# Kernel tuning notes

Hardware: AMD Instinct MI355X
Metric: run time of the kernel (lower is better)

## Reference

```python
import jax, jax.numpy as jnp
import numpy as np

# --- placement constants (mirror init_kwargs) ---
N = 500_000           # total nodes
M = 450_000           # movable nodes (first M)
NBX = 1024
NBY = 1024
XL = 0.0
YL = 0.0
BSX = 1.0
BSY = 1.0
K = 8                 # max bin span per axis for 'large' nodes (node size < 7*bin)


def setup_inputs() -> dict:
    key = jax.random.key(0)
    k1, k2, k3, k4, k5, k6 = jax.random.split(key, 6)
    # node centers strictly inside the die so large-node windows stay in range
    px = jax.random.uniform(k1, (N,), jnp.float32, 4.0, 1020.0)
    py = jax.random.uniform(k2, (N,), jnp.float32, 4.0, 1020.0)
    pos = jnp.concatenate([px, py])                      # [2N]
    potential_field = jax.random.normal(k3, (NBX, NBY), jnp.float32)
    rho_current = jax.random.uniform(k4, (NBX, NBY), jnp.float32, 0.1, 2.0)
    node_size_x = jax.random.uniform(k5, (N,), jnp.float32, 0.2, 6.0)
    node_size_y = jax.random.uniform(k6, (N,), jnp.float32, 0.2, 6.0)
    return {"pos": pos, "potential_field": potential_field,
            "rho_current": rho_current,
            "node_size_x": node_size_x, "node_size_y": node_size_y}


def _velocity_field(pot, hx, hy):
    # v = -grad(phi): 2nd-order central interior, 1st-order one-sided edges
    vx = -jnp.concatenate([(pot[1:2] - pot[0:1]) / hx,
                           (pot[2:] - pot[:-2]) / (2.0 * hx),
                           (pot[-1:] - pot[-2:-1]) / hx], axis=0)
    vy = -jnp.concatenate([(pot[:, 1:2] - pot[:, 0:1]) / hy,
                           (pot[:, 2:] - pot[:, :-2]) / (2.0 * hy),
                           (pot[:, -1:] - pot[:, -2:-1]) / hy], axis=1)
    return vx, vy


def _axis_window(center, size, lo, bs, nb):
    # per-node K-bin window of overlap lengths along one axis
    left = center - 0.5 * size
    right = center + 0.5 * size
    bmin = jnp.clip(jnp.floor((left - lo) / bs).astype(jnp.int32), 0, nb - 1)
    bmax = jnp.clip(jnp.floor((right - lo) / bs).astype(jnp.int32), 0, nb - 1)
    b = bmin[:, None] + jnp.arange(K, dtype=jnp.int32)        # [M,K]
    bin_left = lo + b.astype(jnp.float32) * bs
    ov = jnp.minimum(right[:, None], bin_left + bs) - jnp.maximum(left[:, None], bin_left)
    ov = jnp.where((b <= bmax[:, None]) & (ov > 0.0), ov, 0.0)
    return jnp.clip(b, 0, nb - 1), ov


def _interpolate_flux(pos, flux_x, flux_y, nsx, nsy):
    pos_x = pos[:N]
    pos_y = pos[N:]
    px = pos_x[:M]
    py = pos_y[:M]
    # --- bilinear path (small nodes) ---
    gx = (px - XL) / BSX
    gy = (py - YL) / BSY
    ix = jnp.clip(jnp.floor(gx).astype(jnp.int32), 0, NBX - 1)
    iy = jnp.clip(jnp.floor(gy).astype(jnp.int32), 0, NBY - 1)
    wx = jnp.clip(gx - ix.astype(jnp.float32), 0.0, 1.0)
    wy = jnp.clip(gy - iy.astype(jnp.float32), 0.0, 1.0)
    ix1 = jnp.clip(ix + 1, 0, NBX - 1)
    iy1 = jnp.clip(iy + 1, 0, NBY - 1)

    def bilerp(f):
        return ((1.0 - wx) * (1.0 - wy) * f[ix, iy] + wx * (1.0 - wy) * f[ix1, iy]
                + (1.0 - wx) * wy * f[ix, iy1] + wx * wy * f[ix1, iy1])

    bil_fx = bilerp(flux_x)
    bil_fy = bilerp(flux_y)
    # --- exact area-weighted path (large nodes), vectorized over K x K window ---
    w = nsx[:M]
    h = nsy[:M]
    bx, ox = _axis_window(px, w, XL, BSX, NBX)                # [M,K]
    by, oy = _axis_window(py, h, YL, BSY, NBY)                # [M,K]
    weights = ox[:, :, None] * oy[:, None, :]                 # [M,K,K] overlap areas
    fx_win = flux_x[bx[:, :, None], by[:, None, :]]           # [M,K,K]
    fy_win = flux_y[bx[:, :, None], by[:, None, :]]
    area = w * h
    safe_area = jnp.maximum(area, 1e-30)
    area_fx = jnp.where(area > 0.0, (fx_win * weights).sum((1, 2)) / safe_area, 0.0)
    area_fy = jnp.where(area > 0.0, (fy_win * weights).sum((1, 2)) / safe_area, 0.0)
    large = (w >= BSX) | (h >= BSY)
    gpx = jnp.where(large, area_fx, bil_fx)
    gpy = jnp.where(large, area_fy, bil_fy)
    grad_pos = jnp.zeros_like(pos)
    grad_pos = grad_pos.at[:M].set(gpx)
    grad_pos = grad_pos.at[N:N + M].set(gpy)
    return grad_pos


def reference(pos, potential_field, rho_current, node_size_x, node_size_y):
    vx, vy = _velocity_field(potential_field, BSX, BSY)
    bin_area = BSX * BSY
    energy = 0.5 * (rho_current * bin_area * (vx * vx + vy * vy)).sum().reshape(1)
    grad_pos = _interpolate_flux(pos, vx, vy, node_size_x, node_size_y)
    return energy, grad_pos
```

## Files before the change

kernel.cpp:

```cpp
#include <hip/hip_runtime.h>
#include <hip/hip_fp16.h>

#define NPART 500000
#define MPART 450000
#define NBXC 1024
#define NBYC 1024
#define KROW 7
#define NBLK_PART 1954

__global__ __launch_bounds__(256) void field_kernel(const float* __restrict__ pot,
                                                    const float* __restrict__ rho,
                                                    __half2* __restrict__ v,
                                                    float* __restrict__ partials) {
    const int idx = blockIdx.x * 256 + threadIdx.x;
    const int i  = idx >> 8;
    const int j4 = (idx & 255) << 2;

    const int ip = min(i + 1, NBXC - 1);
    const int im = max(i - 1, 0);
    const float sx = (ip - im == 2) ? 0.5f : 1.0f;

    const float4 c  = *reinterpret_cast<const float4*>(pot + i  * NBYC + j4);
    const float4 cu = *reinterpret_cast<const float4*>(pot + ip * NBYC + j4);
    const float4 cd = *reinterpret_cast<const float4*>(pot + im * NBYC + j4);
    const float  cl = pot[i * NBYC + max(j4 - 1, 0)];
    const float  cr = pot[i * NBYC + min(j4 + 4, NBYC - 1)];
    const float4 r4 = *reinterpret_cast<const float4*>(rho + i * NBYC + j4);

    const float vx0 = -(cu.x - cd.x) * sx;
    const float vx1 = -(cu.y - cd.y) * sx;
    const float vx2 = -(cu.z - cd.z) * sx;
    const float vx3 = -(cu.w - cd.w) * sx;

    const float vy0 = (j4 == 0)             ? -(c.y - c.x) : -(c.y - cl) * 0.5f;
    const float vy1 = -(c.z - c.x) * 0.5f;
    const float vy2 = -(c.w - c.y) * 0.5f;
    const float vy3 = (j4 + 3 == NBYC - 1)  ? -(c.w - c.z) : -(cr - c.z) * 0.5f;

    float4 st;
    st.x = __builtin_bit_cast(float, __floats2half2_rn(vx0, vy0));
    st.y = __builtin_bit_cast(float, __floats2half2_rn(vx1, vy1));
    st.z = __builtin_bit_cast(float, __floats2half2_rn(vx2, vy2));
    st.w = __builtin_bit_cast(float, __floats2half2_rn(vx3, vy3));
    *reinterpret_cast<float4*>(v + i * NBYC + j4) = st;

    float e = r4.x * (vx0 * vx0 + vy0 * vy0)
            + r4.y * (vx1 * vx1 + vy1 * vy1)
            + r4.z * (vx2 * vx2 + vy2 * vy2)
            + r4.w * (vx3 * vx3 + vy3 * vy3);
    #pragma unroll
    for (int off = 32; off > 0; off >>= 1) e += __shfl_down(e, off, 64);
    __shared__ float smem[4];
    const int lane = threadIdx.x & 63;
    const int wid  = threadIdx.x >> 6;
    if (lane == 0) smem[wid] = e;
    __syncthreads();
    if (threadIdx.x == 0) partials[blockIdx.x] = (smem[0] + smem[1]) + (smem[2] + smem[3]);
}

__global__ __launch_bounds__(256) void particle_kernel(const float* __restrict__ pos,
                                                       const float* __restrict__ nsx,
                                                       const float* __restrict__ nsy,
                                                       const __half2* __restrict__ v,
                                                       const float* __restrict__ partials,
                                                       float* __restrict__ out) {
    __shared__ float smem[4];

    if (blockIdx.x == NBLK_PART) {
        const int t = threadIdx.x;
        float e = (partials[t] + partials[t + 256]) + (partials[t + 512] + partials[t + 768]);
        #pragma unroll
        for (int off = 32; off > 0; off >>= 1) e += __shfl_down(e, off, 64);
        const int lane = t & 63;
        const int wid  = t >> 6;
        if (lane == 0) smem[wid] = e;
        __syncthreads();
        if (t == 0) out[0] = 0.5f * ((smem[0] + smem[1]) + (smem[2] + smem[3]));
        return;
    }

    const int i = blockIdx.x * 256 + threadIdx.x;
    if (i >= NPART) return;
    if (i >= MPART) {
        out[1 + i]         = 0.0f;
        out[1 + NPART + i] = 0.0f;
        return;
    }

    const float px = pos[i];
    const float py = pos[NPART + i];
    const float w  = nsx[i];
    const float h  = nsy[i];

    float gpx, gpy;
    const bool large = (w >= 1.0f) || (h >= 1.0f);
    if (!large) {
        int ix = min(max((int)floorf(px), 0), NBXC - 1);
        int iy = min(max((int)floorf(py), 0), NBYC - 1);
        const float wx = fminf(fmaxf(px - (float)ix, 0.0f), 1.0f);
        const float wy = fminf(fmaxf(py - (float)iy, 0.0f), 1.0f);
        const int ix1 = min(ix + 1, NBXC - 1);
        const int iy1 = min(iy + 1, NBYC - 1);
        const float2 f00 = __half22float2(v[ix  * NBYC + iy ]);
        const float2 f10 = __half22float2(v[ix1 * NBYC + iy ]);
        const float2 f01 = __half22float2(v[ix  * NBYC + iy1]);
        const float2 f11 = __half22float2(v[ix1 * NBYC + iy1]);
        const float w00 = (1.0f - wx) * (1.0f - wy);
        const float w10 = wx * (1.0f - wy);
        const float w01 = (1.0f - wx) * wy;
        const float w11 = wx * wy;
        gpx = w00 * f00.x + w10 * f10.x + w01 * f01.x + w11 * f11.x;
        gpy = w00 * f00.y + w10 * f10.y + w01 * f01.y + w11 * f11.y;
    } else {
        const float lx = px - 0.5f * w, rx = px + 0.5f * w;
        const float ly = py - 0.5f * h, ry = py + 0.5f * h;
        const int bminx = min(max((int)floorf(lx), 0), NBXC - 1);
        const int bmaxx = min(max((int)floorf(rx), 0), NBXC - 1);
        const int bminy = min(max((int)floorf(ly), 0), NBYC - 1);
        const int bmaxy = min(max((int)floorf(ry), 0), NBYC - 1);
        const int by0 = min(bminy & ~3, NBYC - 12);
        const int nax = bmaxx - bminx;
        const bool need3 = (bmaxy >= by0 + 8);

        float4 q[KROW][3];
        #pragma unroll
        for (int k = 0; k < KROW; ++k) {
            const int bx = bminx + min(k, nax);
            const float4* rp = reinterpret_cast<const float4*>(v + bx * NBYC + by0);
            q[k][0] = rp[0];
            q[k][1] = rp[1];
            q[k][2] = need3 ? rp[2] : make_float4(0.0f, 0.0f, 0.0f, 0.0f);
        }

        float oy[12];
        #pragma unroll
        for (int k = 0; k < 12; ++k) {
            const int b = by0 + k;
            const float bl = (float)b;
            float ov = fminf(ry, bl + 1.0f) - fmaxf(ly, bl);
            oy[k] = (b <= bmaxy && ov > 0.0f) ? ov : 0.0f;
        }
        float ox[KROW];
        #pragma unroll
        for (int k = 0; k < KROW; ++k) {
            const int b = bminx + k;
            const float bl = (float)b;
            float ov = fminf(rx, bl + 1.0f) - fmaxf(lx, bl);
            ox[k] = (b <= bmaxx && ov > 0.0f) ? ov : 0.0f;
        }

        float afx = 0.0f, afy = 0.0f;
        #pragma unroll
        for (int k = 0; k < KROW; ++k) {
            float sx = 0.0f, sy = 0.0f;
            #pragma unroll
            for (int r = 0; r < 3; ++r) {
                const float* qs = &q[k][r].x;
                #pragma unroll
                for (int e = 0; e < 4; ++e) {
                    const float2 f = __half22float2(__builtin_bit_cast(__half2, qs[e]));
                    sx += f.x * oy[r * 4 + e];
                    sy += f.y * oy[r * 4 + e];
                }
            }
            afx += sx * ox[k];
            afy += sy * ox[k];
        }
        const float inv = 1.0f / fmaxf(w * h, 1e-30f);
        gpx = afx * inv;
        gpy = afy * inv;
    }
    out[1 + i]         = gpx;
    out[1 + NPART + i] = gpy;
}

extern "C" void kernel_launch(void* const* d_in, const int* in_sizes, int n_in,
                              void* d_out, int out_size, void* d_ws, size_t ws_size,
                              hipStream_t stream) {
    const float* pos = (const float*)d_in[0];
    const float* pot = (const float*)d_in[1];
    const float* rho = (const float*)d_in[2];
    const float* nsx = (const float*)d_in[3];
    const float* nsy = (const float*)d_in[4];
    float* out = (float*)d_out;

    __half2* v      = (__half2*)d_ws;
    float* partials = (float*)((char*)d_ws + (size_t)NBXC * NBYC * sizeof(__half2));

    field_kernel<<<(NBXC * NBYC / 4) / 256, 256, 0, stream>>>(pot, rho, v, partials);
    particle_kernel<<<NBLK_PART + 1, 256, 0, stream>>>(pos, nsx, nsy, v, partials, out);
}
```

Baseline: 35.33 us.

## Store velocity field in 2x8 tiled layout and gather large-node windows by tile

The half2 velocity field is now written in a tiled layout where each 2-row by 8-column block is contiguous, and the field kernel processes 8 columns per thread, halving the block count and the partial-sum count. Large-node area interpolation loads whole 2x8 or 2x16 tiles per pair of x-rows and skips x-pairs with zero overlap, instead of reading 7 separate rows. The aim is better cache-line locality and fewer memory transactions for the windowed gathers. The trade-off is fetching wider aligned windows (up to 8x16) that include unused bins, plus extra index arithmetic for bilinear lookups.

Result: faster. 30.01 us (-15.0%).

```diff
diff --git a/kernel.cpp b/kernel.cpp
--- a/kernel.cpp
+++ b/kernel.cpp
@@ -5,49 +5,57 @@
 #define MPART 450000
 #define NBXC 1024
 #define NBYC 1024
-#define KROW 7
 #define NBLK_PART 1954
+#define NPARTIAL 512
+
+__device__ __forceinline__ int tidx(int x, int y) {
+    return ((((x >> 1) * 128 + (y >> 3)) << 4) + ((x & 1) << 3) + (y & 7));
+}
 
 __global__ __launch_bounds__(256) void field_kernel(const float* __restrict__ pot,
                                                     const float* __restrict__ rho,
                                                     __half2* __restrict__ v,
                                                     float* __restrict__ partials) {
     const int idx = blockIdx.x * 256 + threadIdx.x;
-    const int i  = idx >> 8;
-    const int j4 = (idx & 255) << 2;
-
-    const int ip = min(i + 1, NBXC - 1);
-    const int im = max(i - 1, 0);
+    const int x  = idx >> 7;
+    const int ty = idx & 127;
+    const int j0 = ty << 3;
+
+    const int ip = min(x + 1, NBXC - 1);
+    const int im = max(x - 1, 0);
     const float sx = (ip - im == 2) ? 0.5f : 1.0f;
 
-    const float4 c  = *reinterpret_cast<const float4*>(pot + i  * NBYC + j4);
-    const float4 cu = *reinterpret_cast<const float4*>(pot + ip * NBYC + j4);
-    const float4 cd = *reinterpret_cast<const float4*>(pot + im * NBYC + j4);
-    const float  cl = pot[i * NBYC + max(j4 - 1, 0)];
-    const float  cr = pot[i * NBYC + min(j4 + 4, NBYC - 1)];
-    const float4 r4 = *reinterpret_cast<const float4*>(rho + i * NBYC + j4);
-
-    const float vx0 = -(cu.x - cd.x) * sx;
-    const float vx1 = -(cu.y - cd.y) * sx;
-    const float vx2 = -(cu.z - cd.z) * sx;
-    const float vx3 = -(cu.w - cd.w) * sx;
-
-    const float vy0 = (j4 == 0)             ? -(c.y - c.x) : -(c.y - cl) * 0.5f;
-    const float vy1 = -(c.z - c.x) * 0.5f;
-    const float vy2 = -(c.w - c.y) * 0.5f;
-    const float vy3 = (j4 + 3 == NBYC - 1)  ? -(c.w - c.z) : -(cr - c.z) * 0.5f;
-
-    float4 st;
-    st.x = __builtin_bit_cast(float, __floats2half2_rn(vx0, vy0));
-    st.y = __builtin_bit_cast(float, __floats2half2_rn(vx1, vy1));
-    st.z = __builtin_bit_cast(float, __floats2half2_rn(vx2, vy2));
-    st.w = __builtin_bit_cast(float, __floats2half2_rn(vx3, vy3));
-    *reinterpret_cast<float4*>(v + i * NBYC + j4) = st;
-
-    float e = r4.x * (vx0 * vx0 + vy0 * vy0)
-            + r4.y * (vx1 * vx1 + vy1 * vy1)
-            + r4.z * (vx2 * vx2 + vy2 * vy2)
-            + r4.w * (vx3 * vx3 + vy3 * vy3);
+    const float4* pc = reinterpret_cast<const float4*>(pot + x  * NBYC + j0);
+    const float4* pu = reinterpret_cast<const float4*>(pot + ip * NBYC + j0);
+    const float4* pd = reinterpret_cast<const float4*>(pot + im * NBYC + j0);
+    const float4* pr = reinterpret_cast<const float4*>(rho + x  * NBYC + j0);
+    float c[8], u[8], d[8], r[8];
+    *reinterpret_cast<float4*>(c)     = pc[0]; *reinterpret_cast<float4*>(c + 4) = pc[1];
+    *reinterpret_cast<float4*>(u)     = pu[0]; *reinterpret_cast<float4*>(u + 4) = pu[1];
+    *reinterpret_cast<float4*>(d)     = pd[0]; *reinterpret_cast<float4*>(d + 4) = pd[1];
+    *reinterpret_cast<float4*>(r)     = pr[0]; *reinterpret_cast<float4*>(r + 4) = pr[1];
+    const float cl = pot[x * NBYC + max(j0 - 1, 0)];
+    const float cr = pot[x * NBYC + min(j0 + 8, NBYC - 1)];
+
+    float vx[8], vy[8];
+    #pragma unroll
+    for (int k = 0; k < 8; ++k) vx[k] = -(u[k] - d[k]) * sx;
+    vy[0] = (j0 == 0) ? -(c[1] - c[0]) : -(c[1] - cl) * 0.5f;
+    #pragma unroll
+    for (int k = 1; k < 7; ++k) vy[k] = -(c[k + 1] - c[k - 1]) * 0.5f;
+    vy[7] = (j0 + 7 == NBYC - 1) ? -(c[7] - c[6]) : -(cr - c[6]) * 0.5f;
+
+    float st[8];
+    #pragma unroll
+    for (int k = 0; k < 8; ++k)
+        st[k] = __builtin_bit_cast(float, __floats2half2_rn(vx[k], vy[k]));
+    float4* vp = reinterpret_cast<float4*>(v + ((((x >> 1) * 128 + ty) << 4) + ((x & 1) << 3)));
+    vp[0] = *reinterpret_cast<float4*>(st);
+    vp[1] = *reinterpret_cast<float4*>(st + 4);
+
+    float e = 0.0f;
+    #pragma unroll
+    for (int k = 0; k < 8; ++k) e += r[k] * (vx[k] * vx[k] + vy[k] * vy[k]);
     #pragma unroll
     for (int off = 32; off > 0; off >>= 1) e += __shfl_down(e, off, 64);
     __shared__ float smem[4];
@@ -68,7 +76,7 @@
 
     if (blockIdx.x == NBLK_PART) {
         const int t = threadIdx.x;
-        float e = (partials[t] + partials[t + 256]) + (partials[t + 512] + partials[t + 768]);
+        float e = partials[t] + partials[t + 256];
         #pragma unroll
         for (int off = 32; off > 0; off >>= 1) e += __shfl_down(e, off, 64);
         const int lane = t & 63;
@@ -101,10 +109,10 @@
         const float wy = fminf(fmaxf(py - (float)iy, 0.0f), 1.0f);
         const int ix1 = min(ix + 1, NBXC - 1);
         const int iy1 = min(iy + 1, NBYC - 1);
-        const float2 f00 = __half22float2(v[ix  * NBYC + iy ]);
-        const float2 f10 = __half22float2(v[ix1 * NBYC + iy ]);
-        const float2 f01 = __half22float2(v[ix  * NBYC + iy1]);
-        const float2 f11 = __half22float2(v[ix1 * NBYC + iy1]);
+        const float2 f00 = __half22float2(v[tidx(ix,  iy )]);
+        const float2 f10 = __half22float2(v[tidx(ix1, iy )]);
+        const float2 f01 = __half22float2(v[tidx(ix,  iy1)]);
+        const float2 f11 = __half22float2(v[tidx(ix1, iy1)]);
         const float w00 = (1.0f - wx) * (1.0f - wy);
         const float w10 = wx * (1.0f - wy);
         const float w01 = (1.0f - wx) * wy;
@@ -118,53 +126,68 @@
         const int bmaxx = min(max((int)floorf(rx), 0), NBXC - 1);
         const int bminy = min(max((int)floorf(ly), 0), NBYC - 1);
         const int bmaxy = min(max((int)floorf(ry), 0), NBYC - 1);
-        const int by0 = min(bminy & ~3, NBYC - 12);
-        const int nax = bmaxx - bminx;
-        const bool need3 = (bmaxy >= by0 + 8);
-
-        float4 q[KROW][3];
-        #pragma unroll
-        for (int k = 0; k < KROW; ++k) {
-            const int bx = bminx + min(k, nax);
-            const float4* rp = reinterpret_cast<const float4*>(v + bx * NBYC + by0);
-            q[k][0] = rp[0];
-            q[k][1] = rp[1];
-            q[k][2] = need3 ? rp[2] : make_float4(0.0f, 0.0f, 0.0f, 0.0f);
-        }
-
-        float oy[12];
-        #pragma unroll
-        for (int k = 0; k < 12; ++k) {
+        const int by0 = min(bminy & ~7, NBYC - 16);
+        const int ty0 = by0 >> 3;
+        const int bx0 = bminx & ~1;
+        const bool y2 = (bmaxy - by0) >= 8;
+
+        float oy[16];
+        #pragma unroll
+        for (int k = 0; k < 16; ++k) {
             const int b = by0 + k;
             const float bl = (float)b;
             float ov = fminf(ry, bl + 1.0f) - fmaxf(ly, bl);
             oy[k] = (b <= bmaxy && ov > 0.0f) ? ov : 0.0f;
         }
-        float ox[KROW];
-        #pragma unroll
-        for (int k = 0; k < KROW; ++k) {
-            const int b = bminx + k;
+        float ox[8];
+        #pragma unroll
+        for (int k = 0; k < 8; ++k) {
+            const int b = bx0 + k;
             const float bl = (float)b;
             float ov = fminf(rx, bl + 1.0f) - fmaxf(lx, bl);
-            ox[k] = (b <= bmaxx && ov > 0.0f) ? ov : 0.0f;
+            ov = (b <= bmaxx && ov > 0.0f) ? ov : 0.0f;
+            ox[k] = ov;
         }
 
+        const float4 z = make_float4(0.0f, 0.0f, 0.0f, 0.0f);
         float afx = 0.0f, afy = 0.0f;
         #pragma unroll
-        for (int k = 0; k < KROW; ++k) {
-            float sx = 0.0f, sy = 0.0f;
-            #pragma unroll
-            for (int r = 0; r < 3; ++r) {
-                const float* qs = &q[k][r].x;
+        for (int p = 0; p < 4; ++p) {
+            const float ov0 = ox[2 * p], ov1 = ox[2 * p + 1];
+            if (ov0 > 0.0f || ov1 > 0.0f) {
+                const float4* tp = reinterpret_cast<const float4*>(
+                    v + (((((bx0 >> 1) + p) * 128 + ty0) << 4)));
+                float4 A0 = tp[0], A1 = tp[1], B0 = tp[2], B1 = tp[3];
+                float4 A2 = z, A3 = z, B2 = z, B3 = z;
+                if (y2) { A2 = tp[4]; A3 = tp[5]; B2 = tp[6]; B3 = tp[7]; }
+                float sxa = 0.0f, sya = 0.0f, sxb = 0.0f, syb = 0.0f;
+                const float* a0 = &A0.x; const float* a1 = &A1.x;
+                const float* a2 = &A2.x; const float* a3 = &A3.x;
+                const float* b0 = &B0.x; const float* b1 = &B1.x;
+                const float* b2 = &B2.x; const float* b3 = &B3.x;
                 #pragma unroll
                 for (int e = 0; e < 4; ++e) {
-                    const float2 f = __half22float2(__builtin_bit_cast(__half2, qs[e]));
-                    sx += f.x * oy[r * 4 + e];
-                    sy += f.y * oy[r * 4 + e];
+                    float2 f;
+                    f = __half22float2(__builtin_bit_cast(__half2, a0[e]));
+                    sxa += f.x * oy[e];      sya += f.y * oy[e];
+                    f = __half22float2(__builtin_bit_cast(__half2, a1[e]));
+                    sxa += f.x * oy[4 + e];  sya += f.y * oy[4 + e];
+                    f = __half22float2(__builtin_bit_cast(__half2, a2[e]));
+                    sxa += f.x * oy[8 + e];  sya += f.y * oy[8 + e];
+                    f = __half22float2(__builtin_bit_cast(__half2, a3[e]));
+                    sxa += f.x * oy[12 + e]; sya += f.y * oy[12 + e];
+                    f = __half22float2(__builtin_bit_cast(__half2, b0[e]));
+                    sxb += f.x * oy[e];      syb += f.y * oy[e];
+                    f = __half22float2(__builtin_bit_cast(__half2, b1[e]));
+                    sxb += f.x * oy[4 + e];  syb += f.y * oy[4 + e];
+                    f = __half22float2(__builtin_bit_cast(__half2, b2[e]));
+                    sxb += f.x * oy[8 + e];  syb += f.y * oy[8 + e];
+                    f = __half22float2(__builtin_bit_cast(__half2, b3[e]));
+                    sxb += f.x * oy[12 + e]; syb += f.y * oy[12 + e];
                 }
+                afx += sxa * ov0 + sxb * ov1;
+                afy += sya * ov0 + syb * ov1;
             }
-            afx += sx * ox[k];
-            afy += sy * ox[k];
         }
         const float inv = 1.0f / fmaxf(w * h, 1e-30f);
         gpx = afx * inv;
@@ -187,6 +210,6 @@
     __half2* v      = (__half2*)d_ws;
     float* partials = (float*)((char*)d_ws + (size_t)NBXC * NBYC * sizeof(__half2));
 
-    field_kernel<<<(NBXC * NBYC / 4) / 256, 256, 0, stream>>>(pot, rho, v, partials);
+    field_kernel<<<NPARTIAL, 256, 0, stream>>>(pot, rho, v, partials);
     particle_kernel<<<NBLK_PART + 1, 256, 0, stream>>>(pos, nsx, nsy, v, partials, out);
 }
```
